# Kernel optimization log

Measured on AMD Instinct MI355X. Metric: run time of the kernel, lower is better.

## Reference

```python
import jax, jax.numpy as jnp
import numpy as np

D_MODEL = 1024
N_HEADS = 16
D_K = D_MODEL // N_HEADS
EPS = 1e-8


def _l2_rownorm(x):
    # RowNormActivation: normalize each row (last dim) to unit L2 norm
    return x * jax.lax.rsqrt(jnp.sum(x * x, axis=-1, keepdims=True) + EPS)


def setup_inputs() -> dict:
    key = jax.random.key(0)
    ks = jax.random.split(key, 11)
    B, S = 2, 2048
    sc = 1.0 / np.sqrt(D_MODEL)
    inp = {
        "Q": jax.random.normal(ks[0], (B, S, D_MODEL), jnp.float32),
        "K": jax.random.normal(ks[1], (B, S, D_MODEL), jnp.float32),
        "V": jax.random.normal(ks[2], (B, S, D_MODEL), jnp.float32),
        "Wq_w": jax.random.normal(ks[3], (D_MODEL, D_MODEL), jnp.float32) * sc,
        "Wq_b": jnp.zeros((D_MODEL,), jnp.float32),
        "Wk_w": jax.random.normal(ks[4], (D_MODEL, D_MODEL), jnp.float32) * sc,
        "Wk_b": jnp.zeros((D_MODEL,), jnp.float32),
        "Wv_w": jax.random.normal(ks[5], (D_MODEL, D_MODEL), jnp.float32) * sc,
        "Wv_b": jnp.zeros((D_MODEL,), jnp.float32),
        "Wo_w": jax.random.normal(ks[6], (D_MODEL, D_MODEL), jnp.float32) * sc,
        "Wo_b": jnp.zeros((D_MODEL,), jnp.float32),
    }
    return inp


def reference(Q, K, V, Wq_w, Wq_b, Wk_w, Wk_b, Wv_w, Wv_b, Wo_w, Wo_b):
    B, S, _ = Q.shape
    # torch Linear: y = x @ W.T + b
    q = (Q @ Wq_w.T + Wq_b).reshape(B, S, N_HEADS, D_K).transpose(0, 2, 1, 3)
    k = (K @ Wk_w.T + Wk_b).reshape(B, S, N_HEADS, D_K).transpose(0, 2, 1, 3)
    v = (V @ Wv_w.T + Wv_b).reshape(B, S, N_HEADS, D_K).transpose(0, 2, 1, 3)
    qn = _l2_rownorm(q)
    kn = _l2_rownorm(k)
    scores = jnp.einsum("bhqd,bhkd->bhqk", qn, kn)
    attn = scores * scores  # squared similarity, no softmax (dropout=0 / eval)
    out = jnp.einsum("bhqk,bhkd->bhqd", attn, v)
    out = out.transpose(0, 2, 1, 3).reshape(B, S, D_MODEL)
    return out @ Wo_w.T + Wo_b
```

## Files before the change

### kernel.cpp

```cpp
#include <hip/hip_runtime.h>


#define D_MODEL 1024
#define N_HEADS 16
#define D_K     64
#define BATCH   2
#define SEQ     2048
#define M_TOT   (BATCH * SEQ)

typedef short  s16x8 __attribute__((ext_vector_type(8)));
typedef float  f32x4 __attribute__((ext_vector_type(4)));
typedef unsigned short ushort_t;
typedef ushort_t us4 __attribute__((ext_vector_type(4)));

__device__ __forceinline__ ushort_t f2bf(float f) {
    union { float f; unsigned int u; } x; x.f = f;
    unsigned int u = x.u;
    return (ushort_t)((u + 0x7fffu + ((u >> 16) & 1u)) >> 16);
}
__device__ __forceinline__ float bf2f(ushort_t h) {
    union { unsigned int u; float f; } x; x.u = ((unsigned int)h) << 16;
    return x.f;
}

__device__ __forceinline__ void gload_lds16(const ushort_t* g, ushort_t* l) {
    __builtin_amdgcn_global_load_lds(
        (__attribute__((address_space(1))) void*)(ushort_t*)g,
        (__attribute__((address_space(3))) void*)l, 16, 0, 0);
}

struct ConvArgs {
    const float* src[11];
    ushort_t*    dst[11];
    int          n[11];
};

__global__ __launch_bounds__(256) void convert_kernel(ConvArgs a) {
    const int t = blockIdx.y;
    const int i = (blockIdx.x * 256 + threadIdx.x) * 4;
    if (i >= a.n[t]) return;
    const float4 v = *(const float4*)(a.src[t] + i);
    us4 p;
    p[0] = f2bf(v.x); p[1] = f2bf(v.y); p[2] = f2bf(v.z); p[3] = f2bf(v.w);
    *(us4*)(a.dst[t] + i) = p;
}

template <int BM, int MODE>
__device__ __forceinline__ void gemm_body(
    ushort_t* __restrict__ smem,
    const ushort_t* __restrict__ A,
    const ushort_t* __restrict__ W,
    const ushort_t* __restrict__ bias,
    ushort_t* __restrict__ out,
    float* __restrict__ outf,
    int bx, int by)
{
    static_assert(BM == 64 || BM == 128, "");
    constexpr int K  = 1024;
    constexpr int MF = BM / 32;
    ushort_t* Ast = smem;
    ushort_t* Bst = smem + BM * 64;

    const int t    = threadIdx.x;
    const int wave = t >> 6;
    const int lane = t & 63;
    const int quad = lane >> 4;
    const int lc   = lane & 15;
    const int wm   = wave >> 1;
    const int wn   = wave & 1;
    const int m0   = bx * BM;
    const int n0   = by * 128;

    f32x4 acc[MF][4];
    const f32x4 zero = {0.f, 0.f, 0.f, 0.f};
#pragma unroll
    for (int i = 0; i < MF; ++i)
#pragma unroll
        for (int j = 0; j < 4; ++j) acc[i][j] = zero;

    for (int k0 = 0; k0 < K; k0 += 64) {
#pragma unroll
        for (int c = 0; c < MF; ++c) {
            int idx = c * 256 + t;
            int row = idx >> 3, phys = idx & 7;
            int col = (phys ^ (row & 7)) * 8;
            gload_lds16(A + (size_t)(m0 + row) * K + k0 + col, Ast + idx * 8);
        }
#pragma unroll
        for (int c = 0; c < 4; ++c) {
            int idx = c * 256 + t;
            int row = idx >> 3, phys = idx & 7;
            int col = (phys ^ (row & 7)) * 8;
            gload_lds16(W + (size_t)(n0 + row) * K + k0 + col, Bst + idx * 8);
        }
        __syncthreads();
#pragma unroll
        for (int ks = 0; ks < 2; ++ks) {
            const int ph = ((ks * 4 + quad) ^ (lc & 7)) * 8;
            s16x8 a[MF], b[4];
#pragma unroll
            for (int i = 0; i < MF; ++i)
                a[i] = *(const s16x8*)(Ast + (wm * (BM / 2) + i * 16 + lc) * 64 + ph);
#pragma unroll
            for (int i = 0; i < 4; ++i)
                b[i] = *(const s16x8*)(Bst + (wn * 64 + i * 16 + lc) * 64 + ph);
#pragma unroll
            for (int mf = 0; mf < MF; ++mf)
#pragma unroll
                for (int nf = 0; nf < 4; ++nf)
                    acc[mf][nf] = __builtin_amdgcn_mfma_f32_16x16x32_bf16(
                        a[mf], b[nf], acc[mf][nf], 0, 0, 0);
        }
        __syncthreads();
    }

    float bv[4];
#pragma unroll
    for (int nf = 0; nf < 4; ++nf) bv[nf] = bf2f(bias[n0 + wn * 64 + nf * 16 + lc]);

    if (MODE == 0) {
#pragma unroll
        for (int mf = 0; mf < MF; ++mf)
#pragma unroll
            for (int nf = 0; nf < 4; ++nf)
#pragma unroll
                for (int r = 0; r < 4; ++r) {
                    int mg = m0 + wm * (BM / 2) + mf * 16 + quad * 4 + r;
                    int ng = n0 + wn * 64 + nf * 16 + lc;
                    outf[(size_t)mg * D_MODEL + ng] = acc[mf][nf][r] + bv[nf];
                }
    } else if (MODE == 1) {
#pragma unroll
        for (int mf = 0; mf < MF; ++mf)
#pragma unroll
            for (int r = 0; r < 4; ++r) {
                float ss = 0.f;
#pragma unroll
                for (int nf = 0; nf < 4; ++nf) {
                    float v = acc[mf][nf][r] + bv[nf];
                    acc[mf][nf][r] = v;
                    ss += v * v;
                }
                ss += __shfl_xor(ss, 1);
                ss += __shfl_xor(ss, 2);
                ss += __shfl_xor(ss, 4);
                ss += __shfl_xor(ss, 8);
                float inv = rsqrtf(ss + 1e-8f);
                int mg = m0 + wm * (BM / 2) + mf * 16 + quad * 4 + r;
                int b  = mg >> 11;
                int s  = mg & 2047;
#pragma unroll
                for (int nf = 0; nf < 4; ++nf) {
                    int ng = n0 + wn * 64 + nf * 16 + lc;
                    int h = ng >> 6, d = ng & 63;
                    out[(((size_t)(b * N_HEADS + h)) * SEQ + s) * D_K + d] =
                        f2bf(acc[mf][nf][r] * inv);
                }
            }
    } else {
        ushort_t* vt = smem + wave * (64 * 72);
#pragma unroll
        for (int mf = 0; mf < 4; ++mf)
#pragma unroll
            for (int nf = 0; nf < 4; ++nf) {
                us4 p;
#pragma unroll
                for (int r = 0; r < 4; ++r) p[r] = f2bf(acc[mf][nf][r] + bv[nf]);
                *(us4*)(vt + (nf * 16 + lc) * 72 + mf * 16 + quad * 4) = p;
            }
        asm volatile("s_waitcnt lgkmcnt(0)" ::: "memory");
#pragma unroll
        for (int r = 0; r < 8; ++r) {
            int d  = r * 8 + (lane >> 3);
            int so = (lane & 7) * 8;
            uint4 val = *(const uint4*)(vt + d * 72 + so);
            int mg = m0 + wm * 64 + so;
            int b  = mg >> 11;
            int s  = mg & 2047;
            int ng = n0 + wn * 64 + d;
            int h = ng >> 6, dh = ng & 63;
            *(uint4*)(out + (((size_t)(b * N_HEADS + h)) * D_K + dh) * SEQ + s) = val;
        }
    }
}

__global__ __launch_bounds__(256) void qkv_kernel(
    const ushort_t* __restrict__ Qb, const ushort_t* __restrict__ Kb,
    const ushort_t* __restrict__ Vb,
    const ushort_t* __restrict__ Wq, const ushort_t* __restrict__ Wk,
    const ushort_t* __restrict__ Wv,
    const ushort_t* __restrict__ bq, const ushort_t* __restrict__ bk,
    const ushort_t* __restrict__ bv,
    ushort_t* __restrict__ qn, ushort_t* __restrict__ kn,
    ushort_t* __restrict__ vT)
{
    __shared__ __align__(16) ushort_t smem[4 * 64 * 72];
    const int z = blockIdx.z;
    if (z == 0)
        gemm_body<128, 1>(smem, Qb, Wq, bq, qn, nullptr, blockIdx.x, blockIdx.y);
    else if (z == 1)
        gemm_body<128, 1>(smem, Kb, Wk, bk, kn, nullptr, blockIdx.x, blockIdx.y);
    else
        gemm_body<128, 2>(smem, Vb, Wv, bv, vT, nullptr, blockIdx.x, blockIdx.y);
}

__global__ __launch_bounds__(256) void wo_kernel(
    const ushort_t* __restrict__ A, const ushort_t* __restrict__ W,
    const ushort_t* __restrict__ bias, float* __restrict__ outf)
{
    __shared__ __align__(16) ushort_t smem[(64 + 128) * 64];
    gemm_body<64, 0>(smem, A, W, bias, nullptr, outf, blockIdx.x, blockIdx.y);
}

__global__ __launch_bounds__(256) void attn_kernel(
    const ushort_t* __restrict__ qn,
    const ushort_t* __restrict__ kn,
    const ushort_t* __restrict__ vT,
    ushort_t* __restrict__ attn_out)
{
    __shared__ __align__(16) ushort_t kst[64 * 64];
    __shared__ __align__(16) ushort_t vst[64 * 64];
    __shared__ __align__(16) ushort_t pl_all[4 * 16 * 72];

    const int t    = threadIdx.x;
    const int wave = t >> 6;
    const int lane = t & 63;
    const int quad = lane >> 4;
    const int lc   = lane & 15;
    const int qt   = blockIdx.x;
    const int bh   = blockIdx.y;
    const int b    = bh >> 4;
    const int h    = bh & 15;

    const ushort_t* qb = qn + (size_t)bh * SEQ * D_K;
    const ushort_t* kb = kn + (size_t)bh * SEQ * D_K;
    const ushort_t* vb = vT + (size_t)bh * D_K * SEQ;
    const int q0 = qt * 64 + wave * 16;

    s16x8 aq[2];
#pragma unroll
    for (int ks = 0; ks < 2; ++ks)
        aq[ks] = *(const s16x8*)(qb + (size_t)(q0 + lc) * D_K + ks * 32 + quad * 8);

    f32x4 oacc[4];
    const f32x4 zero = {0.f, 0.f, 0.f, 0.f};
#pragma unroll
    for (int df = 0; df < 4; ++df) oacc[df] = zero;

    ushort_t* pl = pl_all + wave * 16 * 72;

    for (int kt = 0; kt < 32; ++kt) {
        const int j0 = kt * 64;
#pragma unroll
        for (int c = 0; c < 2; ++c) {
            int idx = c * 256 + t;
            int row = idx >> 3, phys = idx & 7;
            int col = (phys ^ (row & 7)) * 8;
            gload_lds16(kb + (size_t)(j0 + row) * D_K + col, kst + idx * 8);
            gload_lds16(vb + (size_t)row * SEQ + j0 + col, vst + idx * 8);
        }
        __syncthreads();

        const int ph0 = ((0 * 4 + quad) ^ (lc & 7)) * 8;
        const int ph1 = ((1 * 4 + quad) ^ (lc & 7)) * 8;
        s16x8 bk[4][2];
#pragma unroll
        for (int jf = 0; jf < 4; ++jf) {
            bk[jf][0] = *(const s16x8*)(kst + (jf * 16 + lc) * 64 + ph0);
            bk[jf][1] = *(const s16x8*)(kst + (jf * 16 + lc) * 64 + ph1);
        }
        f32x4 s[4];
#pragma unroll
        for (int jf = 0; jf < 4; ++jf) {
            s[jf] = zero;
#pragma unroll
            for (int ks = 0; ks < 2; ++ks)
                s[jf] = __builtin_amdgcn_mfma_f32_16x16x32_bf16(aq[ks], bk[jf][ks], s[jf], 0, 0, 0);
        }
        asm volatile("" ::: "memory");
#pragma unroll
        for (int jf = 0; jf < 4; ++jf)
#pragma unroll
            for (int r = 0; r < 4; ++r)
                pl[(quad * 4 + r) * 72 + jf * 16 + lc] = f2bf(s[jf][r] * s[jf][r]);
        s16x8 bvf[4][2];
#pragma unroll
        for (int df = 0; df < 4; ++df) {
            bvf[df][0] = *(const s16x8*)(vst + (df * 16 + lc) * 64 + ph0);
            bvf[df][1] = *(const s16x8*)(vst + (df * 16 + lc) * 64 + ph1);
        }
        asm volatile("s_waitcnt lgkmcnt(0)" ::: "memory");
        s16x8 aa[2];
#pragma unroll
        for (int ks = 0; ks < 2; ++ks)
            aa[ks] = *(const s16x8*)(pl + lc * 72 + ks * 32 + quad * 8);
#pragma unroll
        for (int df = 0; df < 4; ++df)
#pragma unroll
            for (int ks = 0; ks < 2; ++ks)
                oacc[df] = __builtin_amdgcn_mfma_f32_16x16x32_bf16(
                    aa[ks], bvf[df][ks], oacc[df], 0, 0, 0);
        __syncthreads();
    }

#pragma unroll
    for (int df = 0; df < 4; ++df)
#pragma unroll
        for (int r = 0; r < 4; ++r) {
            int s = q0 + quad * 4 + r;
            int d = df * 16 + lc;
            attn_out[((size_t)(b * SEQ + s)) * D_MODEL + h * D_K + d] =
                f2bf(oacc[df][r]);
        }
}

extern "C" void kernel_launch(void* const* d_in, const int* in_sizes, int n_in,
                              void* d_out, int out_size, void* d_ws, size_t ws_size,
                              hipStream_t stream)
{
    const float* Qf   = (const float*)d_in[0];
    const float* Kf   = (const float*)d_in[1];
    const float* Vf   = (const float*)d_in[2];
    const float* Wqf  = (const float*)d_in[3];
    const float* Wqbf = (const float*)d_in[4];
    const float* Wkf  = (const float*)d_in[5];
    const float* Wkbf = (const float*)d_in[6];
    const float* Wvf  = (const float*)d_in[7];
    const float* Wvbf = (const float*)d_in[8];
    const float* Wof  = (const float*)d_in[9];
    const float* Wobf = (const float*)d_in[10];

    const size_t NM = (size_t)M_TOT * D_MODEL;
    const size_t NW = (size_t)D_MODEL * D_MODEL;
    const size_t NB = D_MODEL;

    ushort_t* p = (ushort_t*)d_ws;
    ushort_t* Qb  = p;  p += NM;
    ushort_t* Kb  = p;  p += NM;
    ushort_t* Vb  = p;  p += NM;
    ushort_t* Wq  = p;  p += NW;
    ushort_t* Wk  = p;  p += NW;
    ushort_t* Wv  = p;  p += NW;
    ushort_t* Wo  = p;  p += NW;
    ushort_t* bq  = p;  p += NB;
    ushort_t* bk  = p;  p += NB;
    ushort_t* bvv = p;  p += NB;
    ushort_t* bo  = p;  p += NB;
    ushort_t* qn  = p;  p += NM;
    ushort_t* kn  = p;  p += NM;
    ushort_t* vT  = p;  p += NM;
    ushort_t* ao  = p;  p += NM;

    ConvArgs ca;
    ca.src[0] = Qf;   ca.dst[0] = Qb;  ca.n[0] = (int)NM;
    ca.src[1] = Kf;   ca.dst[1] = Kb;  ca.n[1] = (int)NM;
    ca.src[2] = Vf;   ca.dst[2] = Vb;  ca.n[2] = (int)NM;
    ca.src[3] = Wqf;  ca.dst[3] = Wq;  ca.n[3] = (int)NW;
    ca.src[4] = Wkf;  ca.dst[4] = Wk;  ca.n[4] = (int)NW;
    ca.src[5] = Wvf;  ca.dst[5] = Wv;  ca.n[5] = (int)NW;
    ca.src[6] = Wof;  ca.dst[6] = Wo;  ca.n[6] = (int)NW;
    ca.src[7] = Wqbf; ca.dst[7] = bq;  ca.n[7] = (int)NB;
    ca.src[8] = Wkbf; ca.dst[8] = bk;  ca.n[8] = (int)NB;
    ca.src[9] = Wvbf; ca.dst[9] = bvv; ca.n[9] = (int)NB;
    ca.src[10] = Wobf; ca.dst[10] = bo; ca.n[10] = (int)NB;

    dim3 blk(256);
    convert_kernel<<<dim3((unsigned)(NM / (256 * 4)), 11), blk, 0, stream>>>(ca);

    qkv_kernel<<<dim3(M_TOT / 128, D_MODEL / 128, 3), blk, 0, stream>>>(
        Qb, Kb, Vb, Wq, Wk, Wv, bq, bk, bvv, qn, kn, vT);
    attn_kernel<<<dim3(SEQ / 64, BATCH * N_HEADS), blk, 0, stream>>>(qn, kn, vT, ao);
    wo_kernel<<<dim3(M_TOT / 64, D_MODEL / 128), blk, 0, stream>>>(
        ao, Wo, bo, (float*)d_out);
}
```

Measured before the change: 254.3 us.

## Double-buffer LDS tiles with async global-to-LDS prefetch in GEMM and attention

Both the projection GEMM and the attention loop now keep two LDS buffers and issue global_load_lds for tile it+2 while tile it is computed. Explicit vmcnt waits and s_barrier replace the full __syncthreads, so memory latency overlaps with MFMA work. The cost is twice the LDS per block, which may lower occupancy. The scheme also depends on hand-counted vmcnt values being right, and a wrong count would break correctness.

```diff
diff --git a/kernel.cpp b/kernel.cpp
--- a/kernel.cpp
+++ b/kernel.cpp
@@ -28,6 +28,10 @@
         (__attribute__((address_space(1))) void*)(ushort_t*)g,
         (__attribute__((address_space(3))) void*)l, 16, 0, 0);
 }
+
+#define WAIT_VM(n)  asm volatile("s_waitcnt vmcnt(" #n ")" ::: "memory")
+#define WAIT_LGKM0  asm volatile("s_waitcnt lgkmcnt(0)" ::: "memory")
+#define BARRIER     asm volatile("s_barrier" ::: "memory")
 
 struct ConvArgs {
     const float* src[11];
@@ -56,10 +60,10 @@
     int bx, int by)
 {
     static_assert(BM == 64 || BM == 128, "");
-    constexpr int K  = 1024;
-    constexpr int MF = BM / 32;
-    ushort_t* Ast = smem;
-    ushort_t* Bst = smem + BM * 64;
+    constexpr int K    = 1024;
+    constexpr int MF   = BM / 32;
+    constexpr int BUFW = (BM + 128) * 64;
+    constexpr int NIT  = K / 64;
 
     const int t    = threadIdx.x;
     const int wave = t >> 6;
@@ -78,7 +82,9 @@
 #pragma unroll
         for (int j = 0; j < 4; ++j) acc[i][j] = zero;
 
-    for (int k0 = 0; k0 < K; k0 += 64) {
+    auto stage = [&](int buf, int k0) {
+        ushort_t* Ast = smem + buf * BUFW;
+        ushort_t* Bst = Ast + BM * 64;
 #pragma unroll
         for (int c = 0; c < MF; ++c) {
             int idx = c * 256 + t;
@@ -93,7 +99,10 @@
             int col = (phys ^ (row & 7)) * 8;
             gload_lds16(W + (size_t)(n0 + row) * K + k0 + col, Bst + idx * 8);
         }
-        __syncthreads();
+    };
+    auto comp = [&](int buf) {
+        ushort_t* Ast = smem + buf * BUFW;
+        ushort_t* Bst = Ast + BM * 64;
 #pragma unroll
         for (int ks = 0; ks < 2; ++ks) {
             const int ph = ((ks * 4 + quad) ^ (lc & 7)) * 8;
@@ -111,8 +120,24 @@
                     acc[mf][nf] = __builtin_amdgcn_mfma_f32_16x16x32_bf16(
                         a[mf], b[nf], acc[mf][nf], 0, 0, 0);
         }
-        __syncthreads();
+    };
+
+    stage(0, 0);
+    stage(1, 64);
+    for (int it = 0; it < NIT - 2; ++it) {
+        if constexpr (BM == 128) WAIT_VM(8); else WAIT_VM(6);
+        BARRIER;
+        comp(it & 1);
+        WAIT_LGKM0;
+        BARRIER;
+        stage(it & 1, (it + 2) * 64);
     }
+    if constexpr (BM == 128) WAIT_VM(8); else WAIT_VM(6);
+    BARRIER;
+    comp((NIT - 2) & 1);
+    WAIT_VM(0);
+    BARRIER;
+    comp((NIT - 1) & 1);
 
     float bv[4];
 #pragma unroll
@@ -158,6 +183,7 @@
                 }
             }
     } else {
+        __syncthreads();
         ushort_t* vt = smem + wave * (64 * 72);
 #pragma unroll
         for (int mf = 0; mf < 4; ++mf)
@@ -168,7 +194,7 @@
                 for (int r = 0; r < 4; ++r) p[r] = f2bf(acc[mf][nf][r] + bv[nf]);
                 *(us4*)(vt + (nf * 16 + lc) * 72 + mf * 16 + quad * 4) = p;
             }
-        asm volatile("s_waitcnt lgkmcnt(0)" ::: "memory");
+        WAIT_LGKM0;
 #pragma unroll
         for (int r = 0; r < 8; ++r) {
             int d  = r * 8 + (lane >> 3);
@@ -194,7 +220,7 @@
     ushort_t* __restrict__ qn, ushort_t* __restrict__ kn,
     ushort_t* __restrict__ vT)
 {
-    __shared__ __align__(16) ushort_t smem[4 * 64 * 72];
+    __shared__ __align__(16) ushort_t smem[2 * (128 + 128) * 64];
     const int z = blockIdx.z;
     if (z == 0)
         gemm_body<128, 1>(smem, Qb, Wq, bq, qn, nullptr, blockIdx.x, blockIdx.y);
@@ -208,7 +234,7 @@
     const ushort_t* __restrict__ A, const ushort_t* __restrict__ W,
     const ushort_t* __restrict__ bias, float* __restrict__ outf)
 {
-    __shared__ __align__(16) ushort_t smem[(64 + 128) * 64];
+    __shared__ __align__(16) ushort_t smem[2 * (64 + 128) * 64];
     gemm_body<64, 0>(smem, A, W, bias, nullptr, outf, blockIdx.x, blockIdx.y);
 }
 
@@ -218,9 +244,7 @@
     const ushort_t* __restrict__ vT,
     ushort_t* __restrict__ attn_out)
 {
-    __shared__ __align__(16) ushort_t kst[64 * 64];
-    __shared__ __align__(16) ushort_t vst[64 * 64];
-    __shared__ __align__(16) ushort_t pl_all[4 * 16 * 72];
+    __shared__ __align__(16) ushort_t smem[2 * 8192 + 4 * 16 * 72];
 
     const int t    = threadIdx.x;
     const int wave = t >> 6;
@@ -247,10 +271,11 @@
 #pragma unroll
     for (int df = 0; df < 4; ++df) oacc[df] = zero;
 
-    ushort_t* pl = pl_all + wave * 16 * 72;
-
-    for (int kt = 0; kt < 32; ++kt) {
-        const int j0 = kt * 64;
+    ushort_t* pl = smem + 2 * 8192 + wave * 16 * 72;
+
+    auto stage = [&](int buf, int j0) {
+        ushort_t* kst = smem + buf * 8192;
+        ushort_t* vst = kst + 4096;
 #pragma unroll
         for (int c = 0; c < 2; ++c) {
             int idx = c * 256 + t;
@@ -259,8 +284,10 @@
             gload_lds16(kb + (size_t)(j0 + row) * D_K + col, kst + idx * 8);
             gload_lds16(vb + (size_t)row * SEQ + j0 + col, vst + idx * 8);
         }
-        __syncthreads();
-
+    };
+    auto comp = [&](int buf) {
+        ushort_t* kst = smem + buf * 8192;
+        ushort_t* vst = kst + 4096;
         const int ph0 = ((0 * 4 + quad) ^ (lc & 7)) * 8;
         const int ph1 = ((1 * 4 + quad) ^ (lc & 7)) * 8;
         s16x8 bk[4][2];
@@ -277,7 +304,6 @@
             for (int ks = 0; ks < 2; ++ks)
                 s[jf] = __builtin_amdgcn_mfma_f32_16x16x32_bf16(aq[ks], bk[jf][ks], s[jf], 0, 0, 0);
         }
-        asm volatile("" ::: "memory");
 #pragma unroll
         for (int jf = 0; jf < 4; ++jf)
 #pragma unroll
@@ -289,7 +315,7 @@
             bvf[df][0] = *(const s16x8*)(vst + (df * 16 + lc) * 64 + ph0);
             bvf[df][1] = *(const s16x8*)(vst + (df * 16 + lc) * 64 + ph1);
         }
-        asm volatile("s_waitcnt lgkmcnt(0)" ::: "memory");
+        WAIT_LGKM0;
         s16x8 aa[2];
 #pragma unroll
         for (int ks = 0; ks < 2; ++ks)
@@ -300,8 +326,25 @@
             for (int ks = 0; ks < 2; ++ks)
                 oacc[df] = __builtin_amdgcn_mfma_f32_16x16x32_bf16(
                     aa[ks], bvf[df][ks], oacc[df], 0, 0, 0);
-        __syncthreads();
+    };
+
+    constexpr int NT = 32;
+    stage(0, 0);
+    stage(1, 64);
+    for (int it = 0; it < NT - 2; ++it) {
+        WAIT_VM(4);
+        BARRIER;
+        comp(it & 1);
+        WAIT_LGKM0;
+        BARRIER;
+        stage(it & 1, (it + 2) * 64);
     }
+    WAIT_VM(4);
+    BARRIER;
+    comp((NT - 2) & 1);
+    WAIT_VM(0);
+    BARRIER;
+    comp((NT - 1) & 1);
 
 #pragma unroll
     for (int df = 0; df < 4; ++df)
```

Measured after the change: 238.2 us. -6.3%, faster.
